# Kernel optimization log

Measured on AMD Instinct MI355X. Metric: run time of the kernel, lower is better.

Reference implementation:

```python
import jax, jax.numpy as jnp
import numpy as np

NUM_HEADS = 16


def setup_inputs() -> dict:
    key = jax.random.key(0)
    kq, kk, kv = jax.random.split(key, 3)
    b, s, h = 1, 4096, 1024
    q = jax.random.normal(kq, (b, s, h), dtype=jnp.float32)
    k = jax.random.normal(kk, (b, s, h), dtype=jnp.float32)
    v = jax.random.normal(kv, (b, s, h), dtype=jnp.float32)
    return {"q": q, "k": k, "v": v}


def reference(q, k, v):
    b, s, hd = q.shape
    n = NUM_HEADS
    d = hd // n
    # b s (n d) -> b s n d
    qh = q.reshape(b, s, n, d)
    kh = k.reshape(b, s, n, d)
    vh = v.reshape(b, s, n, d)
    scale = 1.0 / jnp.sqrt(jnp.float32(d))
    # non-causal flash-attention math: softmax(qk^T * scale) v
    scores = jnp.einsum('bqnd,bknd->bnqk', qh, kh) * scale  # [b, n, s, s]
    probs = jax.nn.softmax(scores, axis=-1)
    out = jnp.einsum('bnqk,bknd->bqnd', probs, vh)  # [b, s, n, d]
    return out.reshape(b, s, hd)
```

## Files before the change

### kernel.cpp

```cpp
#include <hip/hip_runtime.h>

#define S_   4096
#define H_   1024
#define NH_  16
#define NT_  64
#define SCALE_LOG2E 0.18033688011112042f

typedef __attribute__((ext_vector_type(8)))  short short8;
typedef __attribute__((ext_vector_type(16))) float f32x16;

__device__ __forceinline__ unsigned short f2bf(float x) {
    union { float f; unsigned u; } c; c.f = x;
    unsigned r = c.u + 0x7fffu + ((c.u >> 16) & 1u);
    return (unsigned short)(r >> 16);
}
__device__ __forceinline__ unsigned pk2(float a, float b) {
    return (unsigned)f2bf(a) | ((unsigned)f2bf(b) << 16);
}
__device__ __forceinline__ unsigned pkt(float a, float b) {
    union { float f; unsigned u; } ca, cb; ca.f = a; cb.f = b;
    return __builtin_amdgcn_perm(cb.u, ca.u, 0x07060302u);
}

__global__ __launch_bounds__(256) void prepack(
    const float* __restrict__ k, const float* __restrict__ v,
    unsigned short* __restrict__ kp, unsigned short* __restrict__ vtp)
{
    const int t  = threadIdx.x;
    const int kt = blockIdx.x, hd = blockIdx.y;
    const size_t tb = ((size_t)hd * NT_ + kt) * 4096;
    uint4* gk = (uint4*)(kp + tb);
    uint4* gv = (uint4*)(vtp + tb);

    #pragma unroll
    for (int it = 0; it < 2; ++it) {
        int idx = t + 256 * it;
        {
            int key = idx >> 3, kc = idx & 7;
            const float* src = k + (size_t)(kt * 64 + key) * H_ + hd * 64 + kc * 8;
            float4 a = *(const float4*)src;
            float4 b = *(const float4*)(src + 4);
            uint4 w;
            w.x = pk2(a.x, a.y); w.y = pk2(a.z, a.w);
            w.z = pk2(b.x, b.y); w.w = pk2(b.z, b.w);
            gk[kc * 64 + key] = w;
        }
        {
            int d = idx & 63, kc = idx >> 6;
            const float* src = v + (size_t)(kt * 64 + kc * 8) * H_ + hd * 64 + d;
            float p[8];
            #pragma unroll
            for (int j = 0; j < 8; ++j) p[j] = src[(size_t)j * H_];
            uint4 w;
            w.x = pk2(p[0], p[1]); w.y = pk2(p[2], p[3]);
            w.z = pk2(p[4], p[5]); w.w = pk2(p[6], p[7]);
            gv[idx] = w;
        }
    }
}

__global__ __launch_bounds__(256, 3) void attn_main(
    const float* __restrict__ q,
    const unsigned short* __restrict__ kp,
    const unsigned short* __restrict__ vtp,
    float* __restrict__ out)
{
    __shared__ __align__(16) float sO[2 * 2048];
    __shared__ float sL[2 * 64];

    const int t   = threadIdx.x;
    const int b   = blockIdx.x;
    const int xcd = b & 7;
    const int bi  = b >> 3;
    const int hd  = xcd * 2 + (bi >> 6);
    const int qt  = bi & 63;

    const int w    = t >> 6;
    const int lane = t & 63;
    const int l31  = lane & 31;
    const int lhi  = lane >> 5;
    const int qh   = w >> 1;
    const int kh   = w & 1;

    const unsigned short* gK = kp  + (size_t)hd * NT_ * 4096;
    const unsigned short* gV = vtp + (size_t)hd * NT_ * 4096;

    short8 qf[4];
    {
        const float* qb = q + (size_t)(qt * 64 + qh * 32 + l31) * H_ + hd * 64 + lhi * 8;
        #pragma unroll
        for (int c = 0; c < 4; ++c) {
            float4 a  = *(const float4*)(qb + c * 16);
            float4 bb = *(const float4*)(qb + c * 16 + 4);
            union { short8 v; unsigned u[4]; } f;
            f.u[0] = pk2(a.x * SCALE_LOG2E, a.y * SCALE_LOG2E);
            f.u[1] = pk2(a.z * SCALE_LOG2E, a.w * SCALE_LOG2E);
            f.u[2] = pk2(bb.x * SCALE_LOG2E, bb.y * SCALE_LOG2E);
            f.u[3] = pk2(bb.z * SCALE_LOG2E, bb.w * SCALE_LOG2E);
            qf[c] = f.v;
        }
    }

    f32x16 Oacc[2];
    #pragma unroll
    for (int h = 0; h < 2; ++h)
        #pragma unroll
        for (int r = 0; r < 16; ++r) Oacc[h][r] = 0.0f;
    float2 ls2; ls2.x = 0.0f; ls2.y = 0.0f;

    const int kOff = (kh * 32 + l31) * 8 + lhi * 512;
    const int vOff = l31 * 8 + (kh * 4 + lhi) * 512;
    const unsigned short* pK = gK + kOff;
    const unsigned short* pV = gV + vOff;

    short8 kfA[4], vfA[4], kfB[4], vfB[4];

#define LOADF(KF, VF, tile)                                                  \
    {                                                                        \
        const unsigned short* kt_ = pK + (size_t)(tile) * 4096;              \
        const unsigned short* vt_ = pV + (size_t)(tile) * 4096;              \
        KF[0] = *(const short8*)(kt_);                                       \
        KF[1] = *(const short8*)(kt_ + 1024);                                \
        KF[2] = *(const short8*)(kt_ + 2048);                                \
        KF[3] = *(const short8*)(kt_ + 3072);                                \
        VF[0] = *(const short8*)(vt_);                                       \
        VF[1] = *(const short8*)(vt_ + 256);                                 \
        VF[2] = *(const short8*)(vt_ + 1024);                                \
        VF[3] = *(const short8*)(vt_ + 1280);                                \
    }

#define COMPUTE(KF, VF)                                                      \
    {                                                                        \
        f32x16 st;                                                           \
        _Pragma("unroll")                                                    \
        for (int r_ = 0; r_ < 16; ++r_) st[r_] = 0.0f;                       \
        st = __builtin_amdgcn_mfma_f32_32x32x16_bf16(KF[0], qf[0], st, 0, 0, 0); \
        st = __builtin_amdgcn_mfma_f32_32x32x16_bf16(KF[1], qf[1], st, 0, 0, 0); \
        st = __builtin_amdgcn_mfma_f32_32x32x16_bf16(KF[2], qf[2], st, 0, 0, 0); \
        st = __builtin_amdgcn_mfma_f32_32x32x16_bf16(KF[3], qf[3], st, 0, 0, 0); \
        unsigned pu[8];                                                      \
        _Pragma("unroll")                                                    \
        for (int i2_ = 0; i2_ < 8; ++i2_) {                                  \
            float p0 = __builtin_amdgcn_exp2f(st[2 * i2_]);                  \
            float p1 = __builtin_amdgcn_exp2f(st[2 * i2_ + 1]);              \
            ls2.x += p0; ls2.y += p1;                                        \
            pu[i2_] = pkt(p0, p1);                                           \
        }                                                                    \
        _Pragma("unroll")                                                    \
        for (int c_ = 0; c_ < 2; ++c_) {                                     \
            unsigned a0 = pu[4 * c_],     b0 = pu[4 * c_ + 2];               \
            unsigned a1 = pu[4 * c_ + 1], b1 = pu[4 * c_ + 3];               \
                                   \
            asm("v_permlane32_swap_b32 %0, %1" : "+v"(a0), "+v"(b0));        \
            asm("v_permlane32_swap_b32 %0, %1" : "+v"(a1), "+v"(b1));        \
            union { short8 v; unsigned u[4]; } pf;                           \
            pf.u[0] = a0; pf.u[1] = a1; pf.u[2] = b0; pf.u[3] = b1;          \
            Oacc[0] = __builtin_amdgcn_mfma_f32_32x32x16_bf16(pf.v, VF[2 * c_],     Oacc[0], 0, 0, 0); \
            Oacc[1] = __builtin_amdgcn_mfma_f32_32x32x16_bf16(pf.v, VF[2 * c_ + 1], Oacc[1], 0, 0, 0); \
        }                                                                    \
    }

    LOADF(kfA, vfA, 0);
    for (int kt2 = 0; kt2 < 31; ++kt2) {
        LOADF(kfB, vfB, 2 * kt2 + 1);
        COMPUTE(kfA, vfA);
        LOADF(kfA, vfA, 2 * kt2 + 2);
        COMPUTE(kfB, vfB);
    }
    LOADF(kfB, vfB, 63);
    COMPUTE(kfA, vfA);
    COMPUTE(kfB, vfB);

#undef LOADF
#undef COMPUTE

    float lsum = ls2.x + ls2.y;
    lsum += __shfl_xor(lsum, 32);
    if (lhi == 0) sL[kh * 64 + qh * 32 + l31] = lsum;
    if (kh == 1) {
        float* o = sO + qh * 2048;
        #pragma unroll
        for (int h = 0; h < 2; ++h)
            #pragma unroll
            for (int r = 0; r < 16; ++r)
                o[h * 1024 + r * 64 + lane] = Oacc[h][r];
    }
    __syncthreads();
    if (kh == 0) {
        float linv[4][4];
        #pragma unroll
        for (int qd = 0; qd < 4; ++qd) {
            int base = qh * 32 + 8 * qd + 4 * lhi;
            float4 a  = *(const float4*)(sL + base);
            float4 bb = *(const float4*)(sL + 64 + base);
            linv[qd][0] = __builtin_amdgcn_rcpf(a.x + bb.x);
            linv[qd][1] = __builtin_amdgcn_rcpf(a.y + bb.y);
            linv[qd][2] = __builtin_amdgcn_rcpf(a.z + bb.z);
            linv[qd][3] = __builtin_amdgcn_rcpf(a.w + bb.w);
        }
        const float* o = sO + qh * 2048;
        #pragma unroll
        for (int h = 0; h < 2; ++h)
            #pragma unroll
            for (int qd = 0; qd < 4; ++qd)
                #pragma unroll
                for (int e = 0; e < 4; ++e) {
                    int r   = 4 * qd + e;
                    int row = qh * 32 + e + 8 * qd + 4 * lhi;
                    float val = (Oacc[h][r] + o[h * 1024 + r * 64 + lane]) * linv[qd][e];
                    out[(size_t)(qt * 64 + row) * H_ + hd * 64 + h * 32 + l31] = val;
                }
    }
}

extern "C" void kernel_launch(void* const* d_in, const int* in_sizes, int n_in,
                              void* d_out, int out_size, void* d_ws, size_t ws_size,
                              hipStream_t stream) {
    const float* q = (const float*)d_in[0];
    const float* k = (const float*)d_in[1];
    const float* v = (const float*)d_in[2];
    float* out = (float*)d_out;

    unsigned short* kp  = (unsigned short*)d_ws;
    unsigned short* vtp = kp + (size_t)NH_ * NT_ * 4096;

    prepack<<<dim3(NT_, NH_), 256, 0, stream>>>(k, v, kp, vtp);
    attn_main<<<dim3(1024), 256, 0, stream>>>(q, kp, vtp, out);
}
```

Measured before the change: 178.6 us.

## Stage prepack through LDS, raise attention occupancy, hoist zero accumulator

The prepack kernel now reads K and V with coalesced float4 loads into padded shared-memory tiles. It then does the K reorder and the V transpose from LDS, replacing the strided per-element global reads of V. The attention kernel's launch bound goes from 3 to 4 waves per SIMD to allow higher occupancy, at the risk of register spills. The zero accumulator for the QK MFMA is hoisted out of the per-tile macro.

```diff
diff --git a/kernel.cpp b/kernel.cpp
--- a/kernel.cpp
+++ b/kernel.cpp
@@ -26,6 +26,9 @@
     const float* __restrict__ k, const float* __restrict__ v,
     unsigned short* __restrict__ kp, unsigned short* __restrict__ vtp)
 {
+    __shared__ unsigned sK[64 * 33];
+    __shared__ unsigned sV[64 * 33];
+
     const int t  = threadIdx.x;
     const int kt = blockIdx.x, hd = blockIdx.y;
     const size_t tb = ((size_t)hd * NT_ + kt) * 4096;
@@ -33,33 +36,53 @@
     uint4* gv = (uint4*)(vtp + tb);
 
     #pragma unroll
-    for (int it = 0; it < 2; ++it) {
-        int idx = t + 256 * it;
-        {
-            int key = idx >> 3, kc = idx & 7;
-            const float* src = k + (size_t)(kt * 64 + key) * H_ + hd * 64 + kc * 8;
-            float4 a = *(const float4*)src;
-            float4 b = *(const float4*)(src + 4);
+    for (int i = 0; i < 4; ++i) {
+        int n   = t + 256 * i;
+        int row = n >> 4, c4 = n & 15;
+        size_t off = (size_t)(kt * 64 + row) * H_ + hd * 64 + c4 * 4;
+        {
+            float4 a = *(const float4*)(k + off);
+            sK[row * 33 + c4 * 2]     = pk2(a.x, a.y);
+            sK[row * 33 + c4 * 2 + 1] = pk2(a.z, a.w);
+        }
+        {
+            float4 a = *(const float4*)(v + off);
+            sV[row * 33 + c4 * 2]     = pk2(a.x, a.y);
+            sV[row * 33 + c4 * 2 + 1] = pk2(a.z, a.w);
+        }
+    }
+    __syncthreads();
+
+    #pragma unroll
+    for (int i = 0; i < 2; ++i) {
+        int o = t + 256 * i;
+        {
+            int kc = o >> 6, key = o & 63;
             uint4 w;
-            w.x = pk2(a.x, a.y); w.y = pk2(a.z, a.w);
-            w.z = pk2(b.x, b.y); w.w = pk2(b.z, b.w);
-            gk[kc * 64 + key] = w;
-        }
-        {
-            int d = idx & 63, kc = idx >> 6;
-            const float* src = v + (size_t)(kt * 64 + kc * 8) * H_ + hd * 64 + d;
-            float p[8];
+            w.x = sK[key * 33 + kc * 4];
+            w.y = sK[key * 33 + kc * 4 + 1];
+            w.z = sK[key * 33 + kc * 4 + 2];
+            w.w = sK[key * 33 + kc * 4 + 3];
+            gk[o] = w;
+        }
+        {
+            int kc = o >> 6, d = o & 63;
+            int dp = d >> 1, sh = (d & 1) * 16;
+            unsigned q[8];
             #pragma unroll
-            for (int j = 0; j < 8; ++j) p[j] = src[(size_t)j * H_];
+            for (int e = 0; e < 8; ++e)
+                q[e] = (sV[(kc * 8 + e) * 33 + dp] >> sh) & 0xffffu;
             uint4 w;
-            w.x = pk2(p[0], p[1]); w.y = pk2(p[2], p[3]);
-            w.z = pk2(p[4], p[5]); w.w = pk2(p[6], p[7]);
-            gv[idx] = w;
-        }
-    }
-}
-
-__global__ __launch_bounds__(256, 3) void attn_main(
+            w.x = q[0] | (q[1] << 16);
+            w.y = q[2] | (q[3] << 16);
+            w.z = q[4] | (q[5] << 16);
+            w.w = q[6] | (q[7] << 16);
+            gv[o] = w;
+        }
+    }
+}
+
+__global__ __launch_bounds__(256, 4) void attn_main(
     const float* __restrict__ q,
     const unsigned short* __restrict__ kp,
     const unsigned short* __restrict__ vtp,
@@ -107,6 +130,10 @@
         #pragma unroll
         for (int r = 0; r < 16; ++r) Oacc[h][r] = 0.0f;
     float2 ls2; ls2.x = 0.0f; ls2.y = 0.0f;
+
+    f32x16 zero16;
+    #pragma unroll
+    for (int r = 0; r < 16; ++r) zero16[r] = 0.0f;
 
     const int kOff = (kh * 32 + l31) * 8 + lhi * 512;
     const int vOff = l31 * 8 + (kh * 4 + lhi) * 512;
@@ -131,10 +158,7 @@
 
 #define COMPUTE(KF, VF)                                                      \
     {                                                                        \
-        f32x16 st;                                                           \
-        _Pragma("unroll")                                                    \
-        for (int r_ = 0; r_ < 16; ++r_) st[r_] = 0.0f;                       \
-        st = __builtin_amdgcn_mfma_f32_32x32x16_bf16(KF[0], qf[0], st, 0, 0, 0); \
+        f32x16 st = __builtin_amdgcn_mfma_f32_32x32x16_bf16(KF[0], qf[0], zero16, 0, 0, 0); \
         st = __builtin_amdgcn_mfma_f32_32x32x16_bf16(KF[1], qf[1], st, 0, 0, 0); \
         st = __builtin_amdgcn_mfma_f32_32x32x16_bf16(KF[2], qf[2], st, 0, 0, 0); \
         st = __builtin_amdgcn_mfma_f32_32x32x16_bf16(KF[3], qf[3], st, 0, 0, 0); \
```

New measurement: 175.5 us. Within noise of the previous version (-1.7%).
